# Kernel tuning notes

Hardware: AMD Instinct MI355X
Metric: run time of the kernel (lower is better)

## Reference

```python
import jax, jax.numpy as jnp
import numpy as np

GAE_GAMMA = 0.99
GAE_LAMBDA = 0.95
T, N_ENVS = 4096, 2048


def setup_inputs() -> dict:
    key = jax.random.key(0)
    k1, k2, k3, k4 = jax.random.split(key, 4)
    rewards = jax.random.normal(k1, (T, N_ENVS), dtype=jnp.float32)
    values = jax.random.normal(k2, (T, N_ENVS), dtype=jnp.float32)
    next_values = jax.random.normal(k3, (T, N_ENVS), dtype=jnp.float32)
    next_dones = jax.random.randint(k4, (T, N_ENVS), 0, 2).astype(jnp.bool_)
    return {"rewards": rewards, "values": values,
            "next_values": next_values, "next_dones": next_dones}


def reference(rewards, values, next_values, next_dones):
    gamma = jnp.asarray(GAE_GAMMA, rewards.dtype)
    lam = jnp.asarray(GAE_LAMBDA, rewards.dtype)
    not_done = 1.0 - next_dones.astype(rewards.dtype)  # ~next_dones
    # deltas[t] = r[t] + gamma * V(s_{t+1}) * ~done[t] - V(s_t)
    deltas = rewards + gamma * next_values * not_done - values
    gae_discount = gamma * lam

    def step(running_gae, inp):
        delta_t, nd_t = inp
        g = delta_t + gae_discount * nd_t * running_gae
        return g, g

    init = jnp.zeros_like(rewards[0])
    # reverse-time scan over the recurrence
    _, adv = jax.lax.scan(step, init, (deltas, not_done), reverse=True)
    returns = adv + values
    return adv, returns
```

## Files before the change

### kernel.cpp

```cpp
#include <hip/hip_runtime.h>

#define TT    4096
#define NENV  2048
#define N2    (NENV / 2)
#define L     8
#define NCH   (TT / L)
#define BPC   4
#define NBLK  (NCH * BPC)

#define GAMMA 0.99f
#define GL    (0.99f * 0.95f)

typedef float v2f __attribute__((ext_vector_type(2)));

#define STEP_AB(r_, v_, nv_, dn_, A_, B_)                    \
    {                                                        \
        const float nd = (dn_) ? 0.0f : 1.0f;                \
        const float di = (r_) + GAMMA * (nv_) * nd - (v_);   \
        const float c  = GL * nd;                            \
        (B_) = di + c * (B_);                                \
        (A_) = c * (A_);                                     \
    }

#define STEP_OUT(r_, v_, nv_, dn_, g_, adv_, ret_)           \
    {                                                        \
        const float nd = (dn_) ? 0.0f : 1.0f;                \
        const float di = (r_) + GAMMA * (nv_) * nd - (v_);   \
        (g_) = di + GL * nd * (g_);                          \
        (adv_) = (g_);                                       \
        (ret_) = (g_) + (v_);                                \
    }

#define P2_PREFETCH(abuf, bbuf, grp_)                        \
    _Pragma("unroll")                                        \
    for (int j = 0; j < 16; ++j) {                           \
        const int c = NCH - 1 - (grp_) * 16 - j;             \
        abuf[j] = As[c * NENV + col];                        \
        bbuf[j] = Bs[c * NENV + col];                        \
    }

#define P2_PROCESS(abuf, bbuf, grp_)                         \
    _Pragma("unroll")                                        \
    for (int j = 0; j < 16; ++j) {                           \
        const int c = NCH - 1 - (grp_) * 16 - j;             \
        Bs[c * NENV + col] = g;      \
        g = fmaf(abuf[j], g, bbuf[j]);                       \
    }

__global__ __launch_bounds__(256, 8) void gae_k1(
    const float2* __restrict__ rp,  const float2* __restrict__ vp,
    const float2* __restrict__ np,  const int2*   __restrict__ dp,
    float2* __restrict__ wsA, float2* __restrict__ wsB)
{
    const int chunk = (int)blockIdx.x >> 2;
    const int c2    = (((int)blockIdx.x & 3) << 8) | (int)threadIdx.x;
    const int base  = chunk * (L * N2) + c2;

    float Ax = 1.f, Ay = 1.f;
    float Bx = 0.f, By = 0.f;
#pragma unroll
    for (int i = L - 1; i >= 0; --i) {
        const int idx   = base + i * N2;
        const float2 r  = rp[idx];
        const float2 v  = vp[idx];
        const float2 nv = np[idx];
        const int2   dn = dp[idx];
        STEP_AB(r.x, v.x, nv.x, dn.x, Ax, Bx);
        STEP_AB(r.y, v.y, nv.y, dn.y, Ay, By);
    }
    wsA[chunk * N2 + c2] = make_float2(Ax, Ay);
    wsB[chunk * N2 + c2] = make_float2(Bx, By);
}

__global__ __launch_bounds__(64) void gae_k2(
    const float* __restrict__ As, float* __restrict__ Bs)
{
    const int col = (int)blockIdx.x * 64 + (int)threadIdx.x;
    float a0[16], b0[16], a1[16], b1[16];
    float g = 0.0f;
    P2_PREFETCH(a0, b0, 0)
    for (int grp = 0; grp < NCH / 16; grp += 2) {
        P2_PREFETCH(a1, b1, grp + 1)
        P2_PROCESS(a0, b0, grp)
        if (grp + 2 < NCH / 16) { P2_PREFETCH(a0, b0, grp + 2) }
        P2_PROCESS(a1, b1, grp + 1)
    }
}

__global__ __launch_bounds__(256, 8) void gae_k3(
    const float2* __restrict__ rp,  const float2* __restrict__ vp,
    const float2* __restrict__ np,  const int2*   __restrict__ dp,
    const float2* __restrict__ gin,
    float2* __restrict__ adv2, float2* __restrict__ ret2)
{
    const int chunk = (int)blockIdx.x >> 2;
    const int c2    = (((int)blockIdx.x & 3) << 8) | (int)threadIdx.x;
    const int base  = chunk * (L * N2) + c2;

    const float2 g0 = gin[chunk * N2 + c2];
    float gx = g0.x, gy = g0.y;
#pragma unroll
    for (int i = L - 1; i >= 0; --i) {
        const int idx   = base + i * N2;
        const float2 r  = rp[idx];
        const float2 v  = vp[idx];
        const float2 nv = np[idx];
        const int2   dn = dp[idx];
        float ax, ay, tx, ty;
        STEP_OUT(r.x, v.x, nv.x, dn.x, gx, ax, tx);
        STEP_OUT(r.y, v.y, nv.y, dn.y, gy, ay, ty);
        v2f av; av.x = ax; av.y = ay;
        v2f tv; tv.x = tx; tv.y = ty;
        __builtin_nontemporal_store(av, (v2f*)&adv2[idx]);
        __builtin_nontemporal_store(tv, (v2f*)&ret2[idx]);
    }
}

extern "C" void kernel_launch(void* const* d_in, const int* in_sizes, int n_in,
                              void* d_out, int out_size, void* d_ws, size_t ws_size,
                              hipStream_t stream) {
    const float2* rp = (const float2*)d_in[0];
    const float2* vp = (const float2*)d_in[1];
    const float2* np = (const float2*)d_in[2];
    const int2*   dp = (const int2*)d_in[3];

    float2* adv2 = (float2*)d_out;
    float2* ret2 = adv2 + (size_t)TT * N2;

    float2* wsA = (float2*)d_ws;
    float2* wsB = wsA + (size_t)NCH * N2;

    gae_k1<<<NBLK, 256, 0, stream>>>(rp, vp, np, dp, wsA, wsB);
    gae_k2<<<NENV / 64, 64, 0, stream>>>((const float*)wsA, (float*)wsB);
    gae_k3<<<NBLK, 256, 0, stream>>>(rp, vp, np, dp, wsB, adv2, ret2);
}
```

Before: 208.9 us.

## Cache deltas as bf16 and done bits as a mask between scan passes

The first pass now writes each delta as bf16 (two packed per word) and the done flags as a 16-bit mask per chunk. The third pass reads these plus values instead of re-reading rewards, next_values and dones in full. This cuts third-pass read traffic, in exchange for extra writes in pass one. Storing deltas in bf16 loses precision in the advantages, which may break accuracy tolerances. The old path stays as a fallback when the workspace is too small.

```diff
diff --git a/kernel.cpp b/kernel.cpp
--- a/kernel.cpp
+++ b/kernel.cpp
@@ -13,6 +13,11 @@
 
 typedef float v2f __attribute__((ext_vector_type(2)));
 
+static __device__ __forceinline__ unsigned bf16_rne(float f) {
+    const unsigned u = __float_as_uint(f);
+    return (u + 0x7FFFu + ((u >> 16) & 1u)) >> 16;
+}
+
 #define STEP_AB(r_, v_, nv_, dn_, A_, B_)                    \
     {                                                        \
         const float nd = (dn_) ? 0.0f : 1.0f;                \
@@ -47,6 +52,74 @@
         g = fmaf(abuf[j], g, bbuf[j]);                       \
     }
 
+__global__ __launch_bounds__(256, 4) void gae_k1s(
+    const float2* __restrict__ rp,  const float2* __restrict__ vp,
+    const float2* __restrict__ np,  const int2*   __restrict__ dp,
+    float2* __restrict__ wsA, float2* __restrict__ wsB,
+    unsigned* __restrict__ dib, unsigned short* __restrict__ msk)
+{
+    const int chunk = (int)blockIdx.x >> 2;
+    const int c2    = (((int)blockIdx.x & 3) << 8) | (int)threadIdx.x;
+    const int base  = chunk * (L * N2) + c2;
+
+    float Ax = 1.f, Ay = 1.f, Bx = 0.f, By = 0.f;
+    unsigned m = 0u;
+#pragma unroll
+    for (int i = L - 1; i >= 0; --i) {
+        const int idx   = base + i * N2;
+        const float2 r  = rp[idx];
+        const float2 v  = vp[idx];
+        const float2 nv = np[idx];
+        const int2   dn = dp[idx];
+        const float ndx = dn.x ? 0.0f : 1.0f;
+        const float dix = r.x + GAMMA * nv.x * ndx - v.x;
+        const float cx  = GL * ndx;
+        Bx = dix + cx * Bx;  Ax = cx * Ax;
+        const float ndy = dn.y ? 0.0f : 1.0f;
+        const float diy = r.y + GAMMA * nv.y * ndy - v.y;
+        const float cy  = GL * ndy;
+        By = diy + cy * By;  Ay = cy * Ay;
+
+        dib[idx] = bf16_rne(dix) | (bf16_rne(diy) << 16);
+        m |= (dn.x ? 1u : 0u) << (2 * i);
+        m |= (dn.y ? 1u : 0u) << (2 * i + 1);
+    }
+    wsA[chunk * N2 + c2] = make_float2(Ax, Ay);
+    wsB[chunk * N2 + c2] = make_float2(Bx, By);
+    msk[chunk * N2 + c2] = (unsigned short)m;
+}
+
+__global__ __launch_bounds__(256, 4) void gae_k3s(
+    const float2* __restrict__ vp,
+    const unsigned* __restrict__ dib, const unsigned short* __restrict__ msk,
+    const float2* __restrict__ gin,
+    float2* __restrict__ adv2, float2* __restrict__ ret2)
+{
+    const int chunk = (int)blockIdx.x >> 2;
+    const int c2    = (((int)blockIdx.x & 3) << 8) | (int)threadIdx.x;
+    const int base  = chunk * (L * N2) + c2;
+
+    const float2 g0 = gin[chunk * N2 + c2];
+    const unsigned m = msk[chunk * N2 + c2];
+    float gx = g0.x, gy = g0.y;
+#pragma unroll
+    for (int i = L - 1; i >= 0; --i) {
+        const int idx = base + i * N2;
+        const unsigned dw = dib[idx];
+        const float dix = __uint_as_float(dw << 16);
+        const float diy = __uint_as_float(dw & 0xFFFF0000u);
+        const float2 v  = vp[idx];
+        const float cx = ((m >> (2 * i)) & 1u) ? 0.0f : GL;
+        const float cy = ((m >> (2 * i + 1)) & 1u) ? 0.0f : GL;
+        gx = dix + cx * gx;
+        gy = diy + cy * gy;
+        v2f a; a.x = gx;       a.y = gy;
+        v2f t; t.x = gx + v.x; t.y = gy + v.y;
+        __builtin_nontemporal_store(a, (v2f*)&adv2[idx]);
+        __builtin_nontemporal_store(t, (v2f*)&ret2[idx]);
+    }
+}
+
 __global__ __launch_bounds__(256, 8) void gae_k1(
     const float2* __restrict__ rp,  const float2* __restrict__ vp,
     const float2* __restrict__ np,  const int2*   __restrict__ dp,
@@ -55,9 +128,7 @@
     const int chunk = (int)blockIdx.x >> 2;
     const int c2    = (((int)blockIdx.x & 3) << 8) | (int)threadIdx.x;
     const int base  = chunk * (L * N2) + c2;
-
-    float Ax = 1.f, Ay = 1.f;
-    float Bx = 0.f, By = 0.f;
+    float Ax = 1.f, Ay = 1.f, Bx = 0.f, By = 0.f;
 #pragma unroll
     for (int i = L - 1; i >= 0; --i) {
         const int idx   = base + i * N2;
@@ -70,6 +141,34 @@
     }
     wsA[chunk * N2 + c2] = make_float2(Ax, Ay);
     wsB[chunk * N2 + c2] = make_float2(Bx, By);
+}
+
+__global__ __launch_bounds__(256, 8) void gae_k3(
+    const float2* __restrict__ rp,  const float2* __restrict__ vp,
+    const float2* __restrict__ np,  const int2*   __restrict__ dp,
+    const float2* __restrict__ gin,
+    float2* __restrict__ adv2, float2* __restrict__ ret2)
+{
+    const int chunk = (int)blockIdx.x >> 2;
+    const int c2    = (((int)blockIdx.x & 3) << 8) | (int)threadIdx.x;
+    const int base  = chunk * (L * N2) + c2;
+    const float2 g0 = gin[chunk * N2 + c2];
+    float gx = g0.x, gy = g0.y;
+#pragma unroll
+    for (int i = L - 1; i >= 0; --i) {
+        const int idx   = base + i * N2;
+        const float2 r  = rp[idx];
+        const float2 v  = vp[idx];
+        const float2 nv = np[idx];
+        const int2   dn = dp[idx];
+        float ax, ay, tx, ty;
+        STEP_OUT(r.x, v.x, nv.x, dn.x, gx, ax, tx);
+        STEP_OUT(r.y, v.y, nv.y, dn.y, gy, ay, ty);
+        v2f av; av.x = ax; av.y = ay;
+        v2f tv; tv.x = tx; tv.y = ty;
+        __builtin_nontemporal_store(av, (v2f*)&adv2[idx]);
+        __builtin_nontemporal_store(tv, (v2f*)&ret2[idx]);
+    }
 }
 
 __global__ __launch_bounds__(64) void gae_k2(
@@ -87,35 +186,6 @@
     }
 }
 
-__global__ __launch_bounds__(256, 8) void gae_k3(
-    const float2* __restrict__ rp,  const float2* __restrict__ vp,
-    const float2* __restrict__ np,  const int2*   __restrict__ dp,
-    const float2* __restrict__ gin,
-    float2* __restrict__ adv2, float2* __restrict__ ret2)
-{
-    const int chunk = (int)blockIdx.x >> 2;
-    const int c2    = (((int)blockIdx.x & 3) << 8) | (int)threadIdx.x;
-    const int base  = chunk * (L * N2) + c2;
-
-    const float2 g0 = gin[chunk * N2 + c2];
-    float gx = g0.x, gy = g0.y;
-#pragma unroll
-    for (int i = L - 1; i >= 0; --i) {
-        const int idx   = base + i * N2;
-        const float2 r  = rp[idx];
-        const float2 v  = vp[idx];
-        const float2 nv = np[idx];
-        const int2   dn = dp[idx];
-        float ax, ay, tx, ty;
-        STEP_OUT(r.x, v.x, nv.x, dn.x, gx, ax, tx);
-        STEP_OUT(r.y, v.y, nv.y, dn.y, gy, ay, ty);
-        v2f av; av.x = ax; av.y = ay;
-        v2f tv; tv.x = tx; tv.y = ty;
-        __builtin_nontemporal_store(av, (v2f*)&adv2[idx]);
-        __builtin_nontemporal_store(tv, (v2f*)&ret2[idx]);
-    }
-}
-
 extern "C" void kernel_launch(void* const* d_in, const int* in_sizes, int n_in,
                               void* d_out, int out_size, void* d_ws, size_t ws_size,
                               hipStream_t stream) {
@@ -130,7 +200,19 @@
     float2* wsA = (float2*)d_ws;
     float2* wsB = wsA + (size_t)NCH * N2;
 
-    gae_k1<<<NBLK, 256, 0, stream>>>(rp, vp, np, dp, wsA, wsB);
-    gae_k2<<<NENV / 64, 64, 0, stream>>>((const float*)wsA, (float*)wsB);
-    gae_k3<<<NBLK, 256, 0, stream>>>(rp, vp, np, dp, wsB, adv2, ret2);
-}
+    const size_t need = ((size_t)8 << 20)
+                      + (size_t)TT * N2 * 4
+                      + (size_t)NCH * N2 * 2;
+
+    if (ws_size >= need) {
+        unsigned*       dib = (unsigned*)((char*)d_ws + ((size_t)8 << 20));
+        unsigned short* msk = (unsigned short*)(dib + (size_t)TT * N2);
+        gae_k1s<<<NBLK, 256, 0, stream>>>(rp, vp, np, dp, wsA, wsB, dib, msk);
+        gae_k2<<<NENV / 64, 64, 0, stream>>>((const float*)wsA, (float*)wsB);
+        gae_k3s<<<NBLK, 256, 0, stream>>>(vp, dib, msk, wsB, adv2, ret2);
+    } else {
+        gae_k1<<<NBLK, 256, 0, stream>>>(rp, vp, np, dp, wsA, wsB);
+        gae_k2<<<NENV / 64, 64, 0, stream>>>((const float*)wsA, (float*)wsB);
+        gae_k3<<<NBLK, 256, 0, stream>>>(rp, vp, np, dp, wsB, adv2, ret2);
+    }
+}
```

Result: faster. 203.2 us (-2.7%).
